# Performance work log

Hardware: AMD Instinct MI355X
Metric: run time of the kernel (lower is better)

Reference implementation:

```python
import jax, jax.numpy as jnp
import numpy as np

B, S, D = 8, 2048, 512
FF = 2048
E = 8

def setup_inputs() -> dict:
    key = jax.random.key(0)
    ks = jax.random.split(key, 7)
    s = 1.0 / np.sqrt(D)
    sf = 1.0 / np.sqrt(FF)
    return {
        "x":  jax.random.normal(ks[0], (B, S, D), dtype=jnp.float32),
        "Wg": jax.random.uniform(ks[1], (D, E), jnp.float32, -s, s),
        "bg": jax.random.uniform(ks[2], (E,), jnp.float32, -s, s),
        "W1": jax.random.uniform(ks[3], (E, D, FF), jnp.float32, -s, s),
        "b1": jax.random.uniform(ks[4], (E, FF), jnp.float32, -s, s),
        "W2": jax.random.uniform(ks[5], (E, FF, D), jnp.float32, -sf, sf),
        "b2": jax.random.uniform(ks[6], (E, D), jnp.float32, -sf, sf),
    }

def reference(x, Wg, bg, W1, b1, W2, b2):
    b, s, d = x.shape
    xf = x.reshape(-1, d)                      # [T, D]
    logits = xf @ Wg + bg                      # [T, E]
    probs = jax.nn.softmax(logits, axis=-1)
    pmax = jnp.max(probs, axis=-1)             # [T]
    routes = jnp.argmax(probs, axis=-1)        # [T] int
    xs = xf * pmax[:, None]                    # scale tokens by router prob
    # per-expert FFN over all tokens, select the routed expert's output
    out_tok = jnp.zeros_like(xf)
    for e in range(E):
        h = jax.nn.relu(xs @ W1[e] + b1[e])    # [T, FF]
        y = h @ W2[e] + b2[e]                  # [T, D]
        out_tok = jnp.where((routes == e)[:, None], y, out_tok)
    # torch.cat of per-expert nonzero-index gathers == tokens stably sorted by expert id
    order = jnp.argsort(routes)                # jnp.argsort is stable
    return out_tok[order].reshape(b, s, d)
```

## Files before the change

### kernel.cpp

```cpp
#include <hip/hip_runtime.h>
#include <hip/hip_bf16.h>

constexpr int TTOK  = 16384;
constexpr int DDIM  = 512;
constexpr int FFDIM = 2048;
constexpr int NEXP  = 8;
constexpr int GB_TOK = 16;
constexpr int NGB    = TTOK / GB_TOK;
constexpr int MAXTILES = TTOK / 128 + NEXP;

typedef __attribute__((ext_vector_type(8))) short short8_t;
typedef __attribute__((ext_vector_type(4))) float f32x4_t;

__device__ __forceinline__ unsigned short f2bf(float f) {
    union { float f; unsigned u; } v; v.f = f;
    return (unsigned short)((v.u + 0x7fffu + ((v.u >> 16) & 1u)) >> 16);
}

__device__ __forceinline__ void gl_lds16(const void* g, void* l) {
    __builtin_amdgcn_global_load_lds(
        (const __attribute__((address_space(1))) void*)g,
        (__attribute__((address_space(3))) void*)l,
        16, 0, 0);
}

__global__ __launch_bounds__(256) void transpose_cvt2(const float* __restrict__ W1,
                                                      const float* __restrict__ W2,
                                                      unsigned short* __restrict__ W1T,
                                                      unsigned short* __restrict__ W2T) {
    __shared__ float tile[32][33];
    int z = blockIdx.z;
    bool isW2 = z >= NEXP;
    int e = isW2 ? z - NEXP : z;
    int R = isW2 ? FFDIM : DDIM;
    int C = isW2 ? DDIM : FFDIM;
    int tilesC = C / 32;
    int t = blockIdx.x;
    int c0 = (t % tilesC) * 32;
    int r0 = (t / tilesC) * 32;
    const float* s = (isW2 ? W2 : W1) + (size_t)e * DDIM * FFDIM;
    unsigned short* d = (isW2 ? W2T : W1T) + (size_t)e * DDIM * FFDIM;
    int tx = threadIdx.x & 31, ty = threadIdx.x >> 5;
    #pragma unroll
    for (int i = 0; i < 4; i++)
        tile[ty + 8 * i][tx] = s[(size_t)(r0 + ty + 8 * i) * C + c0 + tx];
    __syncthreads();
    #pragma unroll
    for (int i = 0; i < 4; i++)
        d[(size_t)(c0 + ty + 8 * i) * R + r0 + tx] = f2bf(tile[tx][ty + 8 * i]);
}

__global__ __launch_bounds__(256) void gate_kernel(const float* __restrict__ x,
                                                   const float* __restrict__ Wg,
                                                   const float* __restrict__ bg,
                                                   int* __restrict__ route,
                                                   float* __restrict__ pmax,
                                                   int* __restrict__ blockCounts) {
    __shared__ int cnt[NEXP];
    __shared__ float bgs[NEXP];
    int tid = threadIdx.x;
    if (tid < NEXP) { cnt[tid] = 0; bgs[tid] = bg[tid]; }
    __syncthreads();
    int wave = tid >> 6, lane = tid & 63;
    float w[8][8];
    #pragma unroll
    for (int jj = 0; jj < 8; jj++) {
        float4 a = *(const float4*)(Wg + (size_t)(lane * 8 + jj) * NEXP);
        float4 b = *(const float4*)(Wg + (size_t)(lane * 8 + jj) * NEXP + 4);
        w[jj][0] = a.x; w[jj][1] = a.y; w[jj][2] = a.z; w[jj][3] = a.w;
        w[jj][4] = b.x; w[jj][5] = b.y; w[jj][6] = b.z; w[jj][7] = b.w;
    }
    int tbase = blockIdx.x * GB_TOK + wave * 4;
    for (int it = 0; it < 4; it++) {
        int t = tbase + it;
        float4 xa = *(const float4*)(x + (size_t)t * DDIM + lane * 8);
        float4 xb = *(const float4*)(x + (size_t)t * DDIM + lane * 8 + 4);
        float xs[8] = {xa.x, xa.y, xa.z, xa.w, xb.x, xb.y, xb.z, xb.w};
        double acc[NEXP];
        #pragma unroll
        for (int e = 0; e < NEXP; e++) acc[e] = 0.0;
        #pragma unroll
        for (int jj = 0; jj < 8; jj++) {
            double xv = (double)xs[jj];
            #pragma unroll
            for (int e = 0; e < NEXP; e++) acc[e] += xv * (double)w[jj][e];
        }
        #pragma unroll
        for (int off = 32; off > 0; off >>= 1) {
            #pragma unroll
            for (int e = 0; e < NEXP; e++) acc[e] += __shfl_down(acc[e], off);
        }
        if (lane == 0) {
            double l[NEXP];
            #pragma unroll
            for (int e = 0; e < NEXP; e++) l[e] = acc[e] + (double)bgs[e];
            int r = 0; double lm = l[0];
            #pragma unroll
            for (int e = 1; e < NEXP; e++) if (l[e] > lm) { lm = l[e]; r = e; }
            double s = 0.0;
            #pragma unroll
            for (int e = 0; e < NEXP; e++) s += exp(l[e] - lm);
            route[t] = r;
            pmax[t] = (float)(1.0 / s);
            atomicAdd(&cnt[r], 1);
        }
    }
    __syncthreads();
    if (tid < NEXP) blockCounts[blockIdx.x * NEXP + tid] = cnt[tid];
}

__global__ __launch_bounds__(1024) void scan_kernel(const int* __restrict__ blockCounts,
                                                    int* __restrict__ blockOffsets,
                                                    int* __restrict__ segPrefix,
                                                    int* __restrict__ tilePrefix) {
    __shared__ int sc[NGB][NEXP];
    __shared__ int base[NEXP + 1];
    int b = threadIdx.x;
    int c[NEXP];
    #pragma unroll
    for (int e = 0; e < NEXP; e++) { c[e] = blockCounts[b * NEXP + e]; sc[b][e] = c[e]; }
    __syncthreads();
    for (int off = 1; off < NGB; off <<= 1) {
        int t[NEXP];
        if (b >= off) {
            #pragma unroll
            for (int e = 0; e < NEXP; e++) t[e] = sc[b - off][e];
        }
        __syncthreads();
        if (b >= off) {
            #pragma unroll
            for (int e = 0; e < NEXP; e++) sc[b][e] += t[e];
        }
        __syncthreads();
    }
    if (b == 0) {
        int s = 0;
        #pragma unroll
        for (int e = 0; e < NEXP; e++) { base[e] = s; s += sc[NGB - 1][e]; }
        base[NEXP] = s;
        for (int e = 0; e <= NEXP; e++) segPrefix[e] = base[e];
        int tp = 0;
        tilePrefix[0] = 0;
        for (int e = 0; e < NEXP; e++) {
            tp += (sc[NGB - 1][e] + 127) / 128;
            tilePrefix[e + 1] = tp;
        }
    }
    __syncthreads();
    #pragma unroll
    for (int e = 0; e < NEXP; e++)
        blockOffsets[b * NEXP + e] = base[e] + sc[b][e] - c[e];
}

__global__ __launch_bounds__(256) void scatter_kernel(const float* __restrict__ x,
                                                      const int* __restrict__ route,
                                                      const float* __restrict__ pmax,
                                                      const int* __restrict__ blockOffsets,
                                                      unsigned short* __restrict__ Xs) {
    __shared__ int dstL[GB_TOK];
    __shared__ float pmL[GB_TOK];
    int tid = threadIdx.x;
    int bb = blockIdx.x;
    if (tid < GB_TOK) {
        int t = bb * GB_TOK + tid;
        int r = route[t];
        unsigned long long ltmask = (tid == 0) ? 0ull : ((~0ull) >> (64 - tid));
        int rank = 0;
        #pragma unroll
        for (int e = 0; e < NEXP; e++) {
            unsigned long long m = __ballot(r == e);
            if (r == e) rank = __popcll(m & ltmask);
        }
        dstL[tid] = blockOffsets[bb * NEXP + r] + rank;
        pmL[tid] = pmax[t];
    }
    __syncthreads();
    int wave = tid >> 6, lane = tid & 63;
    for (int rr = 0; rr < 4; rr++) {
        int rowl = wave * 4 + rr;
        int t = bb * GB_TOK + rowl;
        float pm = pmL[rowl];
        const float4* xr = (const float4*)(x + (size_t)t * DDIM) + lane * 2;
        float4 a = xr[0], b = xr[1];
        union { short8_t v; unsigned short s[8]; } o;
        o.s[0] = f2bf(a.x * pm); o.s[1] = f2bf(a.y * pm);
        o.s[2] = f2bf(a.z * pm); o.s[3] = f2bf(a.w * pm);
        o.s[4] = f2bf(b.x * pm); o.s[5] = f2bf(b.y * pm);
        o.s[6] = f2bf(b.z * pm); o.s[7] = f2bf(b.w * pm);
        *(short8_t*)(Xs + (size_t)dstL[rowl] * DDIM + lane * 8) = o.v;
    }
}

template <bool RELU, int NT, typename OutT>
__global__ __launch_bounds__(256) void gemm_seg(const unsigned short* __restrict__ A,
                                                const unsigned short* __restrict__ Bt,
                                                const float* __restrict__ bias,
                                                OutT* __restrict__ C,
                                                const int* __restrict__ segPrefix,
                                                const int* __restrict__ tilePrefix,
                                                int K, int N) {
    constexpr int MI   = (NT == 128) ? 4 : 2;
    constexpr int BPAN = (NT / 16) * 512;
    int t = blockIdx.y;
    if (t >= tilePrefix[NEXP]) return;
    int e = 0;
    #pragma unroll
    for (int i = 1; i <= NEXP; i++) e += (t >= tilePrefix[i]) ? 1 : 0;
    int seg1 = segPrefix[e + 1];
    int m0 = segPrefix[e] + (t - tilePrefix[e]) * 128;
    int n0 = blockIdx.x * NT;

    __shared__ unsigned short As[2 * 4096];
    __shared__ unsigned short Bs[2 * BPAN];

    int tid = threadIdx.x, wave = tid >> 6, lane = tid & 63;
    const unsigned short* Bte = Bt + (size_t)e * N * K;

    int srow = lane >> 2;
    int sg   = (lane & 3) ^ ((lane >> 2) & 3) ^ ((lane >> 4) & 3);
    int scol = sg * 8;

    f32x4_t acc[MI][4];
    #pragma unroll
    for (int i = 0; i < MI; i++)
        #pragma unroll
        for (int j = 0; j < 4; j++) acc[i][j] = (f32x4_t){0.f, 0.f, 0.f, 0.f};

    int wm = (NT == 128) ? ((wave & 1) * 64) : (wave * 32);
    int wn = (NT == 128) ? ((wave >> 1) * 64) : 0;
    int frow = lane & 15;
    int gr = lane >> 4;
    int fswz = (gr ^ (frow & 3) ^ ((frow >> 2) & 3)) * 8;

    for (int kc = 0; kc < K; kc += 64) {
        #pragma unroll
        for (int p = 0; p < 2; p++) {
            #pragma unroll
            for (int i = 0; i < 2; i++) {
                int reg = wave * 2 + i;
                int arow = m0 + reg * 16 + srow;
                arow = arow < TTOK ? arow : TTOK - 1;
                gl_lds16(A + (size_t)arow * K + kc + p * 32 + scol, &As[p * 4096 + reg * 512]);
            }
            if (NT == 128) {
                #pragma unroll
                for (int i = 0; i < 2; i++) {
                    int reg = wave * 2 + i;
                    int brow = n0 + reg * 16 + srow;
                    gl_lds16(Bte + (size_t)brow * K + kc + p * 32 + scol, &Bs[p * BPAN + reg * 512]);
                }
            } else {
                int reg = wave;
                int brow = n0 + reg * 16 + srow;
                gl_lds16(Bte + (size_t)brow * K + kc + p * 32 + scol, &Bs[p * BPAN + reg * 512]);
            }
        }
        __syncthreads();
        #pragma unroll
        for (int p = 0; p < 2; p++) {
            short8_t af[MI], bfr[4];
            #pragma unroll
            for (int i = 0; i < MI; i++)
                af[i] = *(const short8_t*)&As[p * 4096 + (wm + i * 16 + frow) * 32 + fswz];
            #pragma unroll
            for (int j = 0; j < 4; j++)
                bfr[j] = *(const short8_t*)&Bs[p * BPAN + (wn + j * 16 + frow) * 32 + fswz];
            #pragma unroll
            for (int i = 0; i < MI; i++)
                #pragma unroll
                for (int j = 0; j < 4; j++)
                    acc[i][j] = __builtin_amdgcn_mfma_f32_16x16x32_bf16(af[i], bfr[j], acc[i][j], 0, 0, 0);
        }
        __syncthreads();
    }

    int quad = lane >> 4;
    int colb = lane & 15;
    #pragma unroll
    for (int i = 0; i < MI; i++) {
        #pragma unroll
        for (int j = 0; j < 4; j++) {
            int col = n0 + wn + j * 16 + colb;
            float bv = bias[(size_t)e * N + col];
            #pragma unroll
            for (int r = 0; r < 4; r++) {
                int row = m0 + wm + i * 16 + quad * 4 + r;
                if (row < seg1) {
                    float v = acc[i][j][r] + bv;
                    if (RELU) v = fmaxf(v, 0.0f);
                    if constexpr (sizeof(OutT) == 2) {
                        C[(size_t)row * N + col] = (OutT)f2bf(v);
                    } else {
                        C[(size_t)row * N + col] = v;
                    }
                }
            }
        }
    }
}

extern "C" void kernel_launch(void* const* d_in, const int* in_sizes, int n_in,
                              void* d_out, int out_size, void* d_ws, size_t ws_size,
                              hipStream_t stream) {
    const float* x  = (const float*)d_in[0];
    const float* Wg = (const float*)d_in[1];
    const float* bg = (const float*)d_in[2];
    const float* W1 = (const float*)d_in[3];
    const float* b1 = (const float*)d_in[4];
    const float* W2 = (const float*)d_in[5];
    const float* b2 = (const float*)d_in[6];
    float* out = (float*)d_out;

    char* ws = (char*)d_ws;
    size_t off = 0;
    auto alloc = [&](size_t bytes) -> char* {
        char* p = ws + off;
        off += (bytes + 255) & ~(size_t)255;
        return p;
    };
    unsigned short* W1T = (unsigned short*)alloc((size_t)NEXP * DDIM * FFDIM * 2);
    unsigned short* W2T = (unsigned short*)alloc((size_t)NEXP * DDIM * FFDIM * 2);
    unsigned short* Xs  = (unsigned short*)alloc((size_t)TTOK * DDIM * 2);
    unsigned short* H   = (unsigned short*)alloc((size_t)TTOK * FFDIM * 2);
    int*   route        = (int*)alloc((size_t)TTOK * 4);
    float* pmaxArr      = (float*)alloc((size_t)TTOK * 4);
    int*   blockCounts  = (int*)alloc((size_t)NGB * NEXP * 4);
    int*   blockOffsets = (int*)alloc((size_t)NGB * NEXP * 4);
    int*   segPrefix    = (int*)alloc((size_t)(NEXP + 1) * 4);
    int*   tilePrefix   = (int*)alloc((size_t)(NEXP + 1) * 4);

    transpose_cvt2<<<dim3(1024, 1, 2 * NEXP), 256, 0, stream>>>(W1, W2, W1T, W2T);
    gate_kernel<<<NGB, 256, 0, stream>>>(x, Wg, bg, route, pmaxArr, blockCounts);
    scan_kernel<<<1, NGB, 0, stream>>>(blockCounts, blockOffsets, segPrefix, tilePrefix);
    scatter_kernel<<<NGB, 256, 0, stream>>>(x, route, pmaxArr, blockOffsets, Xs);
    gemm_seg<true, 128, unsigned short><<<dim3(FFDIM / 128, MAXTILES, 1), 256, 0, stream>>>(
        Xs, W1T, b1, H, segPrefix, tilePrefix, DDIM, FFDIM);
    gemm_seg<false, 64, float><<<dim3(DDIM / 64, MAXTILES, 1), 256, 0, stream>>>(
        H, W2T, b2, out, segPrefix, tilePrefix, FFDIM, DDIM);
}
```

Baseline: 344.2 us.

## Unify GEMM to 128x128 tiles, swap grid order, stage bf16 epilogue via LDS

Drops the 64-wide N tile variant so both expert GEMMs use 128x128 tiles, which raises per-block reuse for the second GEMM at the cost of fewer blocks. The grid is reordered so consecutive blocks walk M tiles for a fixed N panel, changing which data stays warm in L2. The bf16 epilogue now stages results through padded LDS and writes 16-byte coalesced rows instead of scattered 2-byte stores, which adds extra barriers.

```diff
diff --git a/kernel.cpp b/kernel.cpp
--- a/kernel.cpp
+++ b/kernel.cpp
@@ -191,7 +191,7 @@
     }
 }
 
-template <bool RELU, int NT, typename OutT>
+template <bool RELU, typename OutT>
 __global__ __launch_bounds__(256) void gemm_seg(const unsigned short* __restrict__ A,
                                                 const unsigned short* __restrict__ Bt,
                                                 const float* __restrict__ bias,
@@ -199,19 +199,17 @@
                                                 const int* __restrict__ segPrefix,
                                                 const int* __restrict__ tilePrefix,
                                                 int K, int N) {
-    constexpr int MI   = (NT == 128) ? 4 : 2;
-    constexpr int BPAN = (NT / 16) * 512;
-    int t = blockIdx.y;
+    int t = blockIdx.x;
     if (t >= tilePrefix[NEXP]) return;
     int e = 0;
     #pragma unroll
     for (int i = 1; i <= NEXP; i++) e += (t >= tilePrefix[i]) ? 1 : 0;
     int seg1 = segPrefix[e + 1];
     int m0 = segPrefix[e] + (t - tilePrefix[e]) * 128;
-    int n0 = blockIdx.x * NT;
+    int n0 = blockIdx.y * 128;
 
     __shared__ unsigned short As[2 * 4096];
-    __shared__ unsigned short Bs[2 * BPAN];
+    __shared__ unsigned short Bs[2 * 4096];
 
     int tid = threadIdx.x, wave = tid >> 6, lane = tid & 63;
     const unsigned short* Bte = Bt + (size_t)e * N * K;
@@ -220,14 +218,14 @@
     int sg   = (lane & 3) ^ ((lane >> 2) & 3) ^ ((lane >> 4) & 3);
     int scol = sg * 8;
 
-    f32x4_t acc[MI][4];
-    #pragma unroll
-    for (int i = 0; i < MI; i++)
+    f32x4_t acc[4][4];
+    #pragma unroll
+    for (int i = 0; i < 4; i++)
         #pragma unroll
         for (int j = 0; j < 4; j++) acc[i][j] = (f32x4_t){0.f, 0.f, 0.f, 0.f};
 
-    int wm = (NT == 128) ? ((wave & 1) * 64) : (wave * 32);
-    int wn = (NT == 128) ? ((wave >> 1) * 64) : 0;
+    int wm = (wave & 1) * 64;
+    int wn = (wave >> 1) * 64;
     int frow = lane & 15;
     int gr = lane >> 4;
     int fswz = (gr ^ (frow & 3) ^ ((frow >> 2) & 3)) * 8;
@@ -241,32 +239,22 @@
                 int arow = m0 + reg * 16 + srow;
                 arow = arow < TTOK ? arow : TTOK - 1;
                 gl_lds16(A + (size_t)arow * K + kc + p * 32 + scol, &As[p * 4096 + reg * 512]);
+                int brow = n0 + reg * 16 + srow;
+                gl_lds16(Bte + (size_t)brow * K + kc + p * 32 + scol, &Bs[p * 4096 + reg * 512]);
             }
-            if (NT == 128) {
-                #pragma unroll
-                for (int i = 0; i < 2; i++) {
-                    int reg = wave * 2 + i;
-                    int brow = n0 + reg * 16 + srow;
-                    gl_lds16(Bte + (size_t)brow * K + kc + p * 32 + scol, &Bs[p * BPAN + reg * 512]);
-                }
-            } else {
-                int reg = wave;
-                int brow = n0 + reg * 16 + srow;
-                gl_lds16(Bte + (size_t)brow * K + kc + p * 32 + scol, &Bs[p * BPAN + reg * 512]);
-            }
         }
         __syncthreads();
         #pragma unroll
         for (int p = 0; p < 2; p++) {
-            short8_t af[MI], bfr[4];
-            #pragma unroll
-            for (int i = 0; i < MI; i++)
+            short8_t af[4], bfr[4];
+            #pragma unroll
+            for (int i = 0; i < 4; i++)
                 af[i] = *(const short8_t*)&As[p * 4096 + (wm + i * 16 + frow) * 32 + fswz];
             #pragma unroll
             for (int j = 0; j < 4; j++)
-                bfr[j] = *(const short8_t*)&Bs[p * BPAN + (wn + j * 16 + frow) * 32 + fswz];
-            #pragma unroll
-            for (int i = 0; i < MI; i++)
+                bfr[j] = *(const short8_t*)&Bs[p * 4096 + (wn + j * 16 + frow) * 32 + fswz];
+            #pragma unroll
+            for (int i = 0; i < 4; i++)
                 #pragma unroll
                 for (int j = 0; j < 4; j++)
                     acc[i][j] = __builtin_amdgcn_mfma_f32_16x16x32_bf16(af[i], bfr[j], acc[i][j], 0, 0, 0);
@@ -276,21 +264,50 @@
 
     int quad = lane >> 4;
     int colb = lane & 15;
-    #pragma unroll
-    for (int i = 0; i < MI; i++) {
-        #pragma unroll
-        for (int j = 0; j < 4; j++) {
-            int col = n0 + wn + j * 16 + colb;
-            float bv = bias[(size_t)e * N + col];
-            #pragma unroll
-            for (int r = 0; r < 4; r++) {
-                int row = m0 + wm + i * 16 + quad * 4 + r;
-                if (row < seg1) {
-                    float v = acc[i][j][r] + bv;
-                    if (RELU) v = fmaxf(v, 0.0f);
-                    if constexpr (sizeof(OutT) == 2) {
-                        C[(size_t)row * N + col] = (OutT)f2bf(v);
-                    } else {
+    float bv[4];
+    #pragma unroll
+    for (int j = 0; j < 4; j++) bv[j] = bias[(size_t)e * N + n0 + wn + j * 16 + colb];
+
+    if constexpr (sizeof(OutT) == 2) {
+        unsigned short* cbuf = As;
+        #pragma unroll
+        for (int p = 0; p < 2; p++) {
+            __syncthreads();
+            if ((wave >> 1) == p) {
+                #pragma unroll
+                for (int i = 0; i < 4; i++)
+                    #pragma unroll
+                    for (int j = 0; j < 4; j++)
+                        #pragma unroll
+                        for (int r = 0; r < 4; r++) {
+                            float v = acc[i][j][r] + bv[j];
+                            if (RELU) v = fmaxf(v, 0.0f);
+                            cbuf[(wm + i * 16 + quad * 4 + r) * 72 + j * 16 + colb] = f2bf(v);
+                        }
+            }
+            __syncthreads();
+            int row = tid >> 1, ch = (tid & 1) * 32;
+            int grow = m0 + row;
+            if (grow < seg1) {
+                #pragma unroll
+                for (int k = 0; k < 4; k++) {
+                    short8_t v = *(const short8_t*)&cbuf[row * 72 + ch + k * 8];
+                    *(short8_t*)&C[(size_t)grow * N + n0 + p * 64 + ch + k * 8] = v;
+                }
+            }
+        }
+    } else {
+        #pragma unroll
+        for (int i = 0; i < 4; i++) {
+            #pragma unroll
+            for (int j = 0; j < 4; j++) {
+                int col = n0 + wn + j * 16 + colb;
+                #pragma unroll
+                for (int r = 0; r < 4; r++) {
+                    int row = m0 + wm + i * 16 + quad * 4 + r;
+                    if (row < seg1) {
+                        float v = acc[i][j][r] + bv[j];
+                        if (RELU) v = fmaxf(v, 0.0f);
                         C[(size_t)row * N + col] = v;
                     }
                 }
@@ -333,8 +350,8 @@
     gate_kernel<<<NGB, 256, 0, stream>>>(x, Wg, bg, route, pmaxArr, blockCounts);
     scan_kernel<<<1, NGB, 0, stream>>>(blockCounts, blockOffsets, segPrefix, tilePrefix);
     scatter_kernel<<<NGB, 256, 0, stream>>>(x, route, pmaxArr, blockOffsets, Xs);
-    gemm_seg<true, 128, unsigned short><<<dim3(FFDIM / 128, MAXTILES, 1), 256, 0, stream>>>(
+    gemm_seg<true, unsigned short><<<dim3(MAXTILES, FFDIM / 128, 1), 256, 0, stream>>>(
         Xs, W1T, b1, H, segPrefix, tilePrefix, DDIM, FFDIM);
-    gemm_seg<false, 64, float><<<dim3(DDIM / 64, MAXTILES, 1), 256, 0, stream>>>(
+    gemm_seg<false, float><<<dim3(MAXTILES, DDIM / 128, 1), 256, 0, stream>>>(
         H, W2T, b2, out, segPrefix, tilePrefix, FFDIM, DDIM);
 }
```

New measurement: 313.4 us. 1.1x faster.
